# Optimization experiments

Measured on AMD Instinct MI355X. Metric: run time of the kernel, lower is better.

Reference implementation:

```python
import jax, jax.numpy as jnp
import numpy as np

H, KV, HD = 16, 8, 128           # heads, kv heads, head_dim
THETA, EPS = 1.0e6, 1e-6         # rope theta, rmsnorm eps
QMAX = 127.0                     # symmetric int8


def qdq(x):
    """Symmetric int8 fake quant-dequant along last dim (per-token / per-out-channel)."""
    s = jnp.maximum(jnp.max(jnp.abs(x), axis=-1, keepdims=True) / QMAX, 1e-8)
    q = jnp.clip(jnp.round(x / s), -QMAX, QMAX) * s
    return x + jax.lax.stop_gradient(q - x)  # STE


def rms_norm(x, w):
    v = jnp.mean(jnp.square(x.astype(jnp.float32)), axis=-1, keepdims=True)
    return (x.astype(jnp.float32) * jax.lax.rsqrt(v + EPS)).astype(x.dtype) * w


def rotate_half(x):
    x1, x2 = jnp.split(x, 2, axis=-1)
    return jnp.concatenate([-x2, x1], axis=-1)


def setup_inputs() -> dict:
    key = jax.random.key(0)
    ks = jax.random.split(key, 6)
    B, S, D = 1, 2048, 2048
    return {
        "hidden_states": jax.random.normal(ks[0], (B, S, D), jnp.float32),
        "Wq": jax.random.normal(ks[1], (H * HD, D), jnp.float32) * 0.02,
        "Wk": jax.random.normal(ks[2], (KV * HD, D), jnp.float32) * 0.02,
        "Wv": jax.random.normal(ks[3], (KV * HD, D), jnp.float32) * 0.02,
        "Wo": jax.random.normal(ks[4], (D, H * HD), jnp.float32) * 0.02,
        "q_norm_w": jnp.ones((HD,), jnp.float32),
        "k_norm_w": jnp.ones((HD,), jnp.float32),
        "position_ids": jnp.arange(S, dtype=jnp.int32)[None, :],
    }


def reference(hidden_states, Wq, Wk, Wv, Wo, q_norm_w, k_norm_w, position_ids):
    B, S, D = hidden_states.shape
    xq = qdq(hidden_states)                                  # per-token act quant (shared input)
    q = (xq @ qdq(Wq).T).reshape(B, S, H, HD).transpose(0, 2, 1, 3)   # [B,H,S,hd]
    k = (xq @ qdq(Wk).T).reshape(B, S, KV, HD).transpose(0, 2, 1, 3)  # [B,KV,S,hd]
    v = (xq @ qdq(Wv).T).reshape(B, S, KV, HD).transpose(0, 2, 1, 3)

    q = rms_norm(q, q_norm_w)
    k = rms_norm(k, k_norm_w)

    # rotary embeddings
    inv = 1.0 / (THETA ** (jnp.arange(0, HD, 2, dtype=jnp.float32) / HD))
    freqs = position_ids.astype(jnp.float32)[..., None] * inv          # [B,S,hd/2]
    emb = jnp.concatenate([freqs, freqs], axis=-1)                     # [B,S,hd]
    cos = jnp.cos(emb)[:, None].astype(q.dtype)                        # [B,1,S,hd]
    sin = jnp.sin(emb)[:, None].astype(q.dtype)
    q = q * cos + rotate_half(q) * sin
    k = k * cos + rotate_half(k) * sin

    # qkt_matmul.quant_x1 / quant_x2
    q = qdq(q)
    k = qdq(k)

    # GQA repeat
    g = H // KV
    k = jnp.repeat(k, g, axis=1)
    v = jnp.repeat(v, g, axis=1)

    scores = jnp.einsum("bhqd,bhkd->bhqk", q, k) * (HD ** -0.5)       # [B,H,S,S]
    causal = jnp.tril(jnp.ones((S, S), bool))
    scores = jnp.where(causal[None, None], scores, jnp.float32(-1e9))
    p = jax.nn.softmax(scores.astype(jnp.float32), axis=-1).astype(q.dtype)

    # pv_matmul.quant_x1 / quant_x2
    p = qdq(p)
    v = qdq(v)
    attn = jnp.einsum("bhqk,bhkd->bhqd", p, v)                        # [B,H,S,hd]
    attn = attn.transpose(0, 2, 1, 3).reshape(B, S, H * HD)
    return qdq(attn) @ qdq(Wo).T
```

## Files before the change

kernel.cpp:

```cpp
#include <hip/hip_runtime.h>
#include <math.h>

#define NH 16
#define NKV 8
#define HDIM 128
#define SEQ 2048
#define DMODEL 2048

typedef int   v4i __attribute__((ext_vector_type(4)));
typedef float v4f __attribute__((ext_vector_type(4)));
typedef __bf16 v8bf __attribute__((ext_vector_type(8)));

static constexpr float SM_SCALE = 0.08838834764831843f;

#define GLOBP(p) (__attribute__((address_space(1))) void*)(p)
#define LDSP(p)  (__attribute__((address_space(3))) void*)(p)
#define ASYNC16(g, l) __builtin_amdgcn_global_load_lds(GLOBP(g), LDSP(l), 16, 0, 0)


__global__ __launch_bounds__(256) void quant_all_k(const float* __restrict__ hidden,
        const float* __restrict__ Wq, const float* __restrict__ Wk,
        const float* __restrict__ Wv, const float* __restrict__ Wo,
        signed char* __restrict__ out, float* __restrict__ scale) {
    int p = blockIdx.x;
    int row0g = p * 16;
    const float* in; int lr0;
    if (row0g < 2048)      { in = hidden; lr0 = row0g; }
    else if (row0g < 4096) { in = Wq; lr0 = row0g - 2048; }
    else if (row0g < 5120) { in = Wk; lr0 = row0g - 4096; }
    else if (row0g < 6144) { in = Wv; lr0 = row0g - 5120; }
    else                   { in = Wo; lr0 = row0g - 6144; }
    const int cols = 2048;
    int tid = threadIdx.x;
    __shared__ float srow[16];
    int r = tid >> 4, l16 = tid & 15;
    const float4* x4 = (const float4*)(in + (size_t)(lr0 + r) * cols);
    float amax = 0.f;
    for (int c4 = l16; c4 < (cols >> 2); c4 += 16) {
        float4 v = x4[c4];
        amax = fmaxf(amax, fmaxf(fmaxf(fabsf(v.x), fabsf(v.y)),
                                 fmaxf(fabsf(v.z), fabsf(v.w))));
    }
#pragma unroll
    for (int m = 1; m <= 8; m <<= 1) amax = fmaxf(amax, __shfl_xor(amax, m));
    if (l16 == 0) {
        float s = fmaxf(amax / 127.0f, 1e-8f);
        srow[r] = s;
        scale[row0g + r] = s;
    }
    __syncthreads();
    int total = (cols >> 4) * 16;
    size_t obase = (size_t)p * 32768;
    for (int idx = tid; idx < total; idx += 256) {
        int f = idx >> 6, q = (idx >> 4) & 3, rr = idx & 15;
        const float* src = in + (size_t)(lr0 + rr) * cols + f * 64 + q * 16;
        float s = srow[rr];
        unsigned int wds[4];
#pragma unroll
        for (int g = 0; g < 4; ++g) {
            float4 v = *(const float4*)(src + g * 4);
            int b0 = (int)fminf(fmaxf(rintf(v.x / s), -127.f), 127.f);
            int b1 = (int)fminf(fmaxf(rintf(v.y / s), -127.f), 127.f);
            int b2 = (int)fminf(fmaxf(rintf(v.z / s), -127.f), 127.f);
            int b3 = (int)fminf(fmaxf(rintf(v.w / s), -127.f), 127.f);
            wds[g] = (b0 & 255) | ((b1 & 255) << 8) | ((b2 & 255) << 16) | ((b3 & 255) << 24);
        }
        *(uint4*)(out + obase + (size_t)idx * 16) =
            make_uint4(wds[0], wds[1], wds[2], wds[3]);
    }
}

__global__ __launch_bounds__(256) void row_quant_k(const float* __restrict__ in,
        signed char* __restrict__ out, float* __restrict__ scale, int cols) {
    int row0 = blockIdx.x * 16;
    int tid = threadIdx.x;
    __shared__ float srow[16];
    int r = tid >> 4, l16 = tid & 15;
    const float4* x4 = (const float4*)(in + (size_t)(row0 + r) * cols);
    float amax = 0.f;
    for (int c4 = l16; c4 < (cols >> 2); c4 += 16) {
        float4 v = x4[c4];
        amax = fmaxf(amax, fmaxf(fmaxf(fabsf(v.x), fabsf(v.y)),
                                 fmaxf(fabsf(v.z), fabsf(v.w))));
    }
#pragma unroll
    for (int m = 1; m <= 8; m <<= 1) amax = fmaxf(amax, __shfl_xor(amax, m));
    if (l16 == 0) {
        float s = fmaxf(amax / 127.0f, 1e-8f);
        srow[r] = s;
        scale[row0 + r] = s;
    }
    __syncthreads();
    int total = (cols >> 4) * 16;
    size_t obase = ((size_t)(row0 >> 4) * (cols >> 6)) << 10;
    for (int idx = tid; idx < total; idx += 256) {
        int f = idx >> 6, q = (idx >> 4) & 3, rr = idx & 15;
        const float* src = in + (size_t)(row0 + rr) * cols + f * 64 + q * 16;
        float s = srow[rr];
        unsigned int wds[4];
#pragma unroll
        for (int g = 0; g < 4; ++g) {
            float4 v = *(const float4*)(src + g * 4);
            int b0 = (int)fminf(fmaxf(rintf(v.x / s), -127.f), 127.f);
            int b1 = (int)fminf(fmaxf(rintf(v.y / s), -127.f), 127.f);
            int b2 = (int)fminf(fmaxf(rintf(v.z / s), -127.f), 127.f);
            int b3 = (int)fminf(fmaxf(rintf(v.w / s), -127.f), 127.f);
            wds[g] = (b0 & 255) | ((b1 & 255) << 8) | ((b2 & 255) << 16) | ((b3 & 255) << 24);
        }
        *(uint4*)(out + obase + (size_t)idx * 16) =
            make_uint4(wds[0], wds[1], wds[2], wds[3]);
    }
}

__global__ __launch_bounds__(256, 2) void gemm_i8_k(const signed char* __restrict__ A,
        const float* __restrict__ sa, const signed char* __restrict__ B,
        const float* __restrict__ sb, float* __restrict__ C, int M, int N, int K) {
    __shared__ __align__(16) signed char lsA[2][8192];
    __shared__ __align__(16) signed char lsB[2][8192];
    int tid = threadIdx.x;
    int w = tid >> 6, l = tid & 63;
    int wr = w >> 1, wc = w & 1;
    int lrow = l & 15;
    int m0 = blockIdx.y * 128, n0 = blockIdx.x * 128;
    int kb6 = K >> 6;
    v4i acc[4][4];
#pragma unroll
    for (int i = 0; i < 4; ++i)
#pragma unroll
        for (int j = 0; j < 4; ++j) acc[i][j] = (v4i){0, 0, 0, 0};

    auto stage = [&](int buf, int k6) {
#pragma unroll
        for (int a = 0; a < 2; ++a) {
            int f = a * 4 + w;
            ASYNC16(A + (((size_t)(((m0 >> 4) + f) * kb6 + k6)) << 10) + l * 16,
                    lsA[buf] + f * 1024);
            ASYNC16(B + (((size_t)(((n0 >> 4) + f) * kb6 + k6)) << 10) + l * 16,
                    lsB[buf] + f * 1024);
        }
    };

    stage(0, 0);
    asm volatile("s_waitcnt vmcnt(0)" ::: "memory");
    __syncthreads();
    int cur = 0;
    for (int t = 0; t < kb6; ++t) {
        if (t + 1 < kb6) stage(cur ^ 1, t + 1);
        v4i af[4], bf[4];
#pragma unroll
        for (int i = 0; i < 4; ++i) af[i] = *(const v4i*)(lsA[cur] + (wr * 4 + i) * 1024 + l * 16);
#pragma unroll
        for (int j = 0; j < 4; ++j) bf[j] = *(const v4i*)(lsB[cur] + (wc * 4 + j) * 1024 + l * 16);
#pragma unroll
        for (int i = 0; i < 4; ++i)
#pragma unroll
            for (int j = 0; j < 4; ++j)
                acc[i][j] = __builtin_amdgcn_mfma_i32_16x16x64_i8(af[i], bf[j], acc[i][j], 0, 0, 0);
        asm volatile("s_waitcnt vmcnt(0)" ::: "memory");
        __syncthreads();
        cur ^= 1;
    }
    int r0 = m0 + wr * 64, c0 = n0 + wc * 64;
    int lg = l >> 4;
    float sbv[4];
#pragma unroll
    for (int j = 0; j < 4; ++j) sbv[j] = sb[c0 + j * 16 + lrow];
#pragma unroll
    for (int i = 0; i < 4; ++i) {
        float4 s4 = *(const float4*)(sa + r0 + i * 16 + lg * 4);
        float sav[4] = {s4.x, s4.y, s4.z, s4.w};
#pragma unroll
        for (int j = 0; j < 4; ++j) {
#pragma unroll
            for (int reg = 0; reg < 4; ++reg) {
                int rr = r0 + i * 16 + lg * 4 + reg;
                C[(size_t)rr * N + c0 + j * 16 + lrow] = (float)acc[i][j][reg] * (sav[reg] * sbv[j]);
            }
        }
    }
}

__global__ void rope_init_k(float* __restrict__ inv_tab) {
    int i = threadIdx.x;
    inv_tab[i] = 1.0f / (float)pow(1.0e6, (double)i / 64.0);
}
__global__ void rope_tab_k(const int* __restrict__ pos_ids, const float* __restrict__ inv_tab,
                           float* __restrict__ ct, float* __restrict__ st) {
    int t = blockIdx.x;
    int fi = threadIdx.x;
    float fr = (float)pos_ids[t] * inv_tab[fi];
    float sn, c;
    sincosf(fr, &sn, &c);
    ct[t * 64 + fi] = c;
    st[t * 64 + fi] = sn;
}

__global__ __launch_bounds__(256) void qkv_post_k(const float* __restrict__ qkv_lin,
        const float* __restrict__ qw, const float* __restrict__ kw,
        const float* __restrict__ ct, const float* __restrict__ st,
        signed char* __restrict__ q_i8, float* __restrict__ sq,
        signed char* __restrict__ k_i8, float* __restrict__ sk,
        float* __restrict__ v_dq) {
    int t = blockIdx.x;
    int wv = threadIdx.x >> 6, l = threadIdx.x & 63;
    const float* row = qkv_lin + (size_t)t * 4096;
    float cth = ct[t * 64 + l];
    float sth = st[t * 64 + l];
    size_t ta0 = (size_t)(((t >> 4) * 2) << 10)
               + (size_t)((((l >> 4) & 3) << 8) + ((t & 15) << 4) + (l & 15));
    for (int slot = wv; slot < 32; slot += 4) {
        float x0 = row[slot * 128 + l];
        float x1 = row[slot * 128 + l + 64];
        if (slot < 24) {
            float ss = x0 * x0 + x1 * x1;
#pragma unroll
            for (int m = 1; m <= 32; m <<= 1) ss += __shfl_xor(ss, m);
            float rs = 1.0f / sqrtf(ss / 128.0f + 1e-6f);
            const float* wn = (slot < 16) ? qw : kw;
            x0 = (x0 * rs) * wn[l];
            x1 = (x1 * rs) * wn[l + 64];
            float nx0 = x0 * cth - x1 * sth;
            float nx1 = x1 * cth + x0 * sth;
            x0 = nx0; x1 = nx1;
        }
        float amax = fmaxf(fabsf(x0), fabsf(x1));
#pragma unroll
        for (int m = 1; m <= 32; m <<= 1) amax = fmaxf(amax, __shfl_xor(amax, m));
        float s = fmaxf(amax / 127.0f, 1e-8f);
        float q0 = fminf(fmaxf(rintf(x0 / s), -127.f), 127.f);
        float q1 = fminf(fmaxf(rintf(x1 / s), -127.f), 127.f);
        if (slot < 16) {
            signed char* dst = q_i8 + (size_t)slot * (SEQ * 128);
            dst[ta0] = (signed char)(int)q0;
            dst[ta0 + 1024] = (signed char)(int)q1;
            if (l == 0) sq[slot * SEQ + t] = s;
        } else if (slot < 24) {
            signed char* dst = k_i8 + (size_t)(slot - 16) * (SEQ * 128);
            dst[ta0] = (signed char)(int)q0;
            dst[ta0 + 1024] = (signed char)(int)q1;
            if (l == 0) sk[(slot - 16) * SEQ + t] = s;
        } else {
            float* dst = v_dq + ((size_t)(slot - 24) * SEQ + t) * HDIM;
            dst[l] = q0 * s;
            dst[l + 64] = q1 * s;
        }
    }
}

__device__ __forceinline__ unsigned int f2bf(float x) {
    unsigned int u = __float_as_uint(x);
    return (u + 0x7fffu + ((u >> 16) & 1u)) >> 16;
}
__device__ __forceinline__ float bf2f(unsigned int h) {
    return __uint_as_float(h << 16);
}

__global__ __launch_bounds__(256) void vt_split_k(const float* __restrict__ v_dq,
        unsigned short* __restrict__ vtT) {
    int kv = blockIdx.y, kb = blockIdx.x;
    int t0 = kb * 64;
    __shared__ float tile[64][132];
    int tid = threadIdx.x;
    const float* src = v_dq + ((size_t)kv * SEQ + t0) * HDIM;
#pragma unroll
    for (int i = 0; i < 8; ++i) {
        int f4 = i * 256 + tid;
        int r = f4 >> 5, c = (f4 & 31) << 2;
        float4 v = *(const float4*)(src + r * HDIM + c);
        tile[r][c] = v.x; tile[r][c + 1] = v.y; tile[r][c + 2] = v.z; tile[r][c + 3] = v.w;
    }
    __syncthreads();
    int d = tid >> 1, th = (tid & 1) * 32;
    size_t base_hi = (size_t)(kv * 2 + 0) * (SEQ * 128);
    size_t base_lo = (size_t)(kv * 2 + 1) * (SEQ * 128);
#pragma unroll
    for (int j = 0; j < 32; j += 2) {
        int tl = th + j;
        float a = tile[tl][d], b = tile[tl + 1][d];
        unsigned int ah = f2bf(a), bh = f2bf(b);
        unsigned int al = f2bf(a - bf2f(ah)), bl = f2bf(b - bf2f(bh));
        int off = kb * 8192 + ((d >> 4) * 2 + ((tl >> 5) & 1)) * 512
                + (((d & 15) + (((tl >> 3) & 3) << 4)) << 3) + (tl & 7);
        *(unsigned int*)(vtT + base_hi + off) = ah | (bh << 16);
        *(unsigned int*)(vtT + base_lo + off) = al | (bl << 16);
    }
}

__global__ __launch_bounds__(256, 4) void attn_p1_k(const signed char* __restrict__ q_i8,
        const float* __restrict__ sq, const signed char* __restrict__ k_i8,
        const float* __restrict__ sk, float* __restrict__ mm) {
    int bx = blockIdx.x, hp = blockIdx.y;
    int qb = 31 - (bx >> 2), c = bx & 3;
    int nch = (qb + 8) >> 3;
    if (c >= nch) return;
    int q0 = qb * 64;
    int kb0 = c * 8, kb1 = min((c + 1) * 8, qb + 1);
    int tid = threadIdx.x, w = tid >> 6, l = tid & 63;
    int lrow = l & 15, lg = l >> 4;
    int h0 = hp * 2, h1 = h0 + 1;

    const signed char* qtA = q_i8 + (size_t)h0 * (SEQ * 128)
                           + ((size_t)((((q0 >> 4) + w) * 2)) << 10) + l * 16;
    const signed char* qtB = qtA + (size_t)(SEQ * 128);
    v4i qfA0 = *(const v4i*)(qtA), qfA1 = *(const v4i*)(qtA + 1024);
    v4i qfB0 = *(const v4i*)(qtB), qfB1 = *(const v4i*)(qtB + 1024);
    float4 sA = *(const float4*)(sq + (size_t)h0 * SEQ + q0 + w * 16 + lg * 4);
    float4 sB = *(const float4*)(sq + (size_t)h1 * SEQ + q0 + w * 16 + lg * 4);
    float sqrA[4] = {sA.x, sA.y, sA.z, sA.w};
    float sqrB[4] = {sB.x, sB.y, sB.z, sB.w};
    const signed char* kbase = k_i8 + (size_t)hp * (SEQ * 128);
    const float* skb = sk + (size_t)hp * SEQ;

    float mA[4], mB[4];
#pragma unroll
    for (int r = 0; r < 4; ++r) { mA[r] = -1e30f; mB[r] = -1e30f; }

    v4i ka[8], kn[8];
    float skc[4], skn[4];
    auto loadK = [&](v4i* dst, float* sdst, int k0) {
#pragma unroll
        for (int f = 0; f < 8; ++f)
            dst[f] = *(const v4i*)(kbase + ((size_t)((k0 >> 4) * 2 + f) << 10) + l * 16);
#pragma unroll
        for (int j = 0; j < 4; ++j) sdst[j] = skb[k0 + j * 16 + lrow];
    };

    loadK(ka, skc, kb0 * 64);
    for (int kb = kb0; kb < kb1; ++kb) {
        if (kb + 1 < kb1) loadK(kn, skn, (kb + 1) * 64);
        int k0 = kb * 64;
        v4i sciA[4], sciB[4];
#pragma unroll
        for (int j = 0; j < 4; ++j) {
            v4i z = {0, 0, 0, 0};
            v4i tA = __builtin_amdgcn_mfma_i32_16x16x64_i8(qfA0, ka[j * 2], z, 0, 0, 0);
            sciA[j] = __builtin_amdgcn_mfma_i32_16x16x64_i8(qfA1, ka[j * 2 + 1], tA, 0, 0, 0);
            v4i tB = __builtin_amdgcn_mfma_i32_16x16x64_i8(qfB0, ka[j * 2], z, 0, 0, 0);
            sciB[j] = __builtin_amdgcn_mfma_i32_16x16x64_i8(qfB1, ka[j * 2 + 1], tB, 0, 0, 0);
        }
#pragma unroll
        for (int reg = 0; reg < 4; ++reg) {
            int r = q0 + w * 16 + lg * 4 + reg;
#pragma unroll
            for (int j = 0; j < 4; ++j) {
                bool ok = (k0 + j * 16 + lrow <= r);
                float ss = skc[j] * SM_SCALE;
                float svA = ((float)sciA[j][reg] * sqrA[reg]) * ss;
                float svB = ((float)sciB[j][reg] * sqrB[reg]) * ss;
                mA[reg] = fmaxf(mA[reg], ok ? svA : -1e30f);
                mB[reg] = fmaxf(mB[reg], ok ? svB : -1e30f);
            }
        }
        if (kb + 1 < kb1) {
#pragma unroll
            for (int f = 0; f < 8; ++f) ka[f] = kn[f];
#pragma unroll
            for (int j = 0; j < 4; ++j) skc[j] = skn[j];
        }
    }
#pragma unroll
    for (int reg = 0; reg < 4; ++reg) {
#pragma unroll
        for (int mask = 1; mask <= 8; mask <<= 1) {
            mA[reg] = fmaxf(mA[reg], __shfl_xor(mA[reg], mask));
            mB[reg] = fmaxf(mB[reg], __shfl_xor(mB[reg], mask));
        }
    }
    if (lrow == 0) {
        size_t bA = ((size_t)(h0 * 32 + qb) * 4 + c) * 64;
        size_t bB = ((size_t)(h1 * 32 + qb) * 4 + c) * 64;
#pragma unroll
        for (int reg = 0; reg < 4; ++reg) {
            mm[bA + w * 16 + lg * 4 + reg] = mA[reg];
            mm[bB + w * 16 + lg * 4 + reg] = mB[reg];
        }
    }
}


__global__ __launch_bounds__(256, 2) void attn_p2_k(const signed char* __restrict__ q_i8,
        const float* __restrict__ sq, const signed char* __restrict__ k_i8,
        const float* __restrict__ sk, const unsigned short* __restrict__ vtT,
        const float* __restrict__ mm, float* __restrict__ attn2, float* __restrict__ pp,
        float* __restrict__ zb) {
    __shared__ __align__(16) unsigned short vlds[2][16384];
    __shared__ __align__(16) signed char klds[8192];
    __shared__ __align__(16) unsigned short plds[4096];
    int bx = blockIdx.x, hp = blockIdx.y;
    int qb = 31 - (bx >> 1), c = bx & 1;
    int nch2 = (qb >= 16) ? 2 : 1;
    if (c >= nch2) return;
    int q0 = qb * 64;
    int kb0 = c * 16, kb1 = min((c + 1) * 16, qb + 1);
    int tid = threadIdx.x, w = tid >> 6, l = tid & 63;
    int lrow = l & 15, lg = l >> 4;
    int h0 = hp * 2, h1 = h0 + 1;

    const signed char* qtA = q_i8 + (size_t)h0 * (SEQ * 128)
                           + ((size_t)((((q0 >> 4) + w) * 2)) << 10) + l * 16;
    const signed char* qtB = qtA + (size_t)(SEQ * 128);
    v4i qfA0 = *(const v4i*)(qtA), qfA1 = *(const v4i*)(qtA + 1024);
    v4i qfB0 = *(const v4i*)(qtB), qfB1 = *(const v4i*)(qtB + 1024);
    float4 sA = *(const float4*)(sq + (size_t)h0 * SEQ + q0 + w * 16 + lg * 4);
    float4 sB = *(const float4*)(sq + (size_t)h1 * SEQ + q0 + w * 16 + lg * 4);
    float sqrA[4] = {sA.x, sA.y, sA.z, sA.w};
    float sqrB[4] = {sB.x, sB.y, sB.z, sB.w};

    int nch1 = (qb + 8) >> 3;
    float mfA[4], mfB[4];
#pragma unroll
    for (int reg = 0; reg < 4; ++reg) {
        int r = w * 16 + lg * 4 + reg;
        float MA = -1e30f, MB = -1e30f;
        for (int c1 = 0; c1 < nch1; ++c1) {
            MA = fmaxf(MA, mm[((size_t)(h0 * 32 + qb) * 4 + c1) * 64 + r]);
            MB = fmaxf(MB, mm[((size_t)(h1 * 32 + qb) * 4 + c1) * 64 + r]);
        }
        mfA[reg] = MA; mfB[reg] = MB;
    }

    const signed char* kbase = k_i8 + (size_t)hp * (SEQ * 128);
    const float* skb = sk + (size_t)hp * SEQ;
    const unsigned short* vt_h = vtT + (size_t)(hp * 2 + 0) * (SEQ * 128);
    const unsigned short* vt_l = vtT + (size_t)(hp * 2 + 1) * (SEQ * 128);

    auto issueV = [&](int kb) {
        unsigned short* vb = &vlds[kb & 1][0];
#pragma unroll
        for (int a = 0; a < 8; ++a) {
            int fv = a * 4 + w;
            int sp_ = fv >> 4, fr = fv & 15;
            const unsigned short* vsrc = (sp_ ? vt_l : vt_h) + kb * 8192 + fr * 512 + l * 8;
            ASYNC16(vsrc, vb + fv * 512);
        }
    };
    auto issueK = [&](int kb) {
#pragma unroll
        for (int a = 0; a < 2; ++a) {
            int f = a * 4 + w;
            ASYNC16(kbase + ((size_t)(kb * 8 + f) << 10) + l * 16, klds + f * 1024);
        }
    };

    v4f accA[8], accB[8];
#pragma unroll
    for (int jd = 0; jd < 8; ++jd) {
        accA[jd] = (v4f){0.f, 0.f, 0.f, 0.f};
        accB[jd] = (v4f){0.f, 0.f, 0.f, 0.f};
    }
    float ztA[4] = {0.f, 0.f, 0.f, 0.f};
    float ztB[4] = {0.f, 0.f, 0.f, 0.f};

    issueV(kb0);
    issueK(kb0);
    asm volatile("s_waitcnt vmcnt(0)" ::: "memory");
    __syncthreads();
    for (int kb = kb0; kb < kb1; ++kb) {
        int k0 = kb * 64;
        v4i ka[8];
#pragma unroll
        for (int f = 0; f < 8; ++f)
            ka[f] = *(const v4i*)(klds + f * 1024 + l * 16);
        float skc[4];
#pragma unroll
        for (int j = 0; j < 4; ++j) skc[j] = skb[k0 + j * 16 + lrow];
        __syncthreads();
        if (kb + 1 < kb1) {
            issueV(kb + 1);
            issueK(kb + 1);
        }
        v4i sciA[4], sciB[4];
#pragma unroll
        for (int j = 0; j < 4; ++j) {
            v4i z = {0, 0, 0, 0};
            v4i tA = __builtin_amdgcn_mfma_i32_16x16x64_i8(qfA0, ka[j * 2], z, 0, 0, 0);
            sciA[j] = __builtin_amdgcn_mfma_i32_16x16x64_i8(qfA1, ka[j * 2 + 1], tA, 0, 0, 0);
            v4i tB = __builtin_amdgcn_mfma_i32_16x16x64_i8(qfB0, ka[j * 2], z, 0, 0, 0);
            sciB[j] = __builtin_amdgcn_mfma_i32_16x16x64_i8(qfB1, ka[j * 2 + 1], tB, 0, 0, 0);
        }
#pragma unroll
        for (int reg = 0; reg < 4; ++reg) {
            int rq = lg * 4 + reg;
            int r = q0 + w * 16 + rq;
#pragma unroll
            for (int j = 0; j < 4; ++j) {
                int cc = j * 16 + lrow;
                float pd = 0.f;
                if (k0 + cc <= r) {
                    float sv = ((float)sciA[j][reg] * (sqrA[reg] * skc[j])) * SM_SCALE;
                    float e = __expf(sv - mfA[reg]);
                    ztA[reg] += e;
                    pd = fminf(rintf(127.0f * e), 127.f);
                }
                plds[(w * 2 + (cc >> 5)) * 512 + (rq + 16 * ((cc >> 3) & 3)) * 8 + (cc & 7)] =
                    (unsigned short)(__float_as_uint(pd) >> 16);
            }
        }
        v8bf pfA0 = *(const v8bf*)(plds + (w * 2 + 0) * 512 + l * 8);
        v8bf pfA1 = *(const v8bf*)(plds + (w * 2 + 1) * 512 + l * 8);
#pragma unroll
        for (int reg = 0; reg < 4; ++reg) {
            int rq = lg * 4 + reg;
            int r = q0 + w * 16 + rq;
#pragma unroll
            for (int j = 0; j < 4; ++j) {
                int cc = j * 16 + lrow;
                float pd = 0.f;
                if (k0 + cc <= r) {
                    float sv = ((float)sciB[j][reg] * (sqrB[reg] * skc[j])) * SM_SCALE;
                    float e = __expf(sv - mfB[reg]);
                    ztB[reg] += e;
                    pd = fminf(rintf(127.0f * e), 127.f);
                }
                plds[(w * 2 + (cc >> 5)) * 512 + (rq + 16 * ((cc >> 3) & 3)) * 8 + (cc & 7)] =
                    (unsigned short)(__float_as_uint(pd) >> 16);
            }
        }
        v8bf pfB0 = *(const v8bf*)(plds + (w * 2 + 0) * 512 + l * 8);
        v8bf pfB1 = *(const v8bf*)(plds + (w * 2 + 1) * 512 + l * 8);
        const unsigned short* vb = &vlds[kb & 1][0];
#pragma unroll
        for (int jd = 0; jd < 8; ++jd) {
            v8bf vh0 = *(const v8bf*)(vb + (jd * 2 + 0) * 512 + l * 8);
            v8bf vh1 = *(const v8bf*)(vb + (jd * 2 + 1) * 512 + l * 8);
            v8bf vl0 = *(const v8bf*)(vb + (16 + jd * 2 + 0) * 512 + l * 8);
            v8bf vl1 = *(const v8bf*)(vb + (16 + jd * 2 + 1) * 512 + l * 8);
            v4f tA = accA[jd];
            tA = __builtin_amdgcn_mfma_f32_16x16x32_bf16(pfA0, vh0, tA, 0, 0, 0);
            tA = __builtin_amdgcn_mfma_f32_16x16x32_bf16(pfA1, vh1, tA, 0, 0, 0);
            tA = __builtin_amdgcn_mfma_f32_16x16x32_bf16(pfA0, vl0, tA, 0, 0, 0);
            tA = __builtin_amdgcn_mfma_f32_16x16x32_bf16(pfA1, vl1, tA, 0, 0, 0);
            accA[jd] = tA;
            v4f tB = accB[jd];
            tB = __builtin_amdgcn_mfma_f32_16x16x32_bf16(pfB0, vh0, tB, 0, 0, 0);
            tB = __builtin_amdgcn_mfma_f32_16x16x32_bf16(pfB1, vh1, tB, 0, 0, 0);
            tB = __builtin_amdgcn_mfma_f32_16x16x32_bf16(pfB0, vl0, tB, 0, 0, 0);
            tB = __builtin_amdgcn_mfma_f32_16x16x32_bf16(pfB1, vl1, tB, 0, 0, 0);
            accB[jd] = tB;
        }
        asm volatile("s_waitcnt vmcnt(0)" ::: "memory");
        __syncthreads();
    }
#pragma unroll
    for (int reg = 0; reg < 4; ++reg) {
#pragma unroll
        for (int mask = 1; mask <= 8; mask <<= 1) {
            ztA[reg] += __shfl_xor(ztA[reg], mask);
            ztB[reg] += __shfl_xor(ztB[reg], mask);
        }
    }
    if (qb < 16) {
        float spA[4], spB[4];
#pragma unroll
        for (int reg = 0; reg < 4; ++reg) {
            spA[reg] = fmaxf((1.0f / ztA[reg]) / 127.0f, 1e-8f);
            spB[reg] = fmaxf((1.0f / ztB[reg]) / 127.0f, 1e-8f);
        }
#pragma unroll
        for (int jd = 0; jd < 8; ++jd)
#pragma unroll
            for (int reg = 0; reg < 4; ++reg) {
                int r = q0 + w * 16 + lg * 4 + reg;
                attn2[(size_t)r * DMODEL + h0 * HDIM + jd * 16 + lrow] = accA[jd][reg] * spA[reg];
                attn2[(size_t)r * DMODEL + h1 * HDIM + jd * 16 + lrow] = accB[jd][reg] * spB[reg];
            }
    } else {
        if (c == 0) {
#pragma unroll
            for (int jd = 0; jd < 8; ++jd)
#pragma unroll
                for (int reg = 0; reg < 4; ++reg) {
                    int r = q0 + w * 16 + lg * 4 + reg;
                    attn2[(size_t)r * DMODEL + h0 * HDIM + jd * 16 + lrow] = accA[jd][reg];
                    attn2[(size_t)r * DMODEL + h1 * HDIM + jd * 16 + lrow] = accB[jd][reg];
                }
        } else {
#pragma unroll
            for (int jd = 0; jd < 8; ++jd)
#pragma unroll
                for (int reg = 0; reg < 4; ++reg) {
                    int rr = w * 16 + lg * 4 + reg;
                    pp[(((size_t)h0 * 16 + (qb - 16)) * 64 + rr) * 128 + jd * 16 + lrow] = accA[jd][reg];
                    pp[(((size_t)h1 * 16 + (qb - 16)) * 64 + rr) * 128 + jd * 16 + lrow] = accB[jd][reg];
                }
        }
        if (lrow == 0) {
            size_t zA = (((size_t)h0 * 16 + (qb - 16)) * 2 + c) * 64;
            size_t zB = (((size_t)h1 * 16 + (qb - 16)) * 2 + c) * 64;
#pragma unroll
            for (int reg = 0; reg < 4; ++reg) {
                zb[zA + w * 16 + lg * 4 + reg] = ztA[reg];
                zb[zB + w * 16 + lg * 4 + reg] = ztB[reg];
            }
        }
    }
}

__global__ __launch_bounds__(256) void attn_red_k(float* __restrict__ attn2,
        const float* __restrict__ pp, const float* __restrict__ zb) {
    int t16 = blockIdx.x, h = blockIdx.y;
    int qb = t16 + 16;
    int tid = threadIdx.x;
    for (int e = tid; e < 2048; e += 256) {
        int i = (e * 4) >> 7, j = (e * 4) & 127;
        float z0 = zb[(((size_t)h * 16 + t16) * 2 + 0) * 64 + i];
        float z1 = zb[(((size_t)h * 16 + t16) * 2 + 1) * 64 + i];
        float zinv = 1.0f / (z0 + z1);
        float spv = fmaxf(zinv / 127.0f, 1e-8f);
        float4 p = *(const float4*)&pp[(((size_t)h * 16 + t16) * 64 + i) * 128 + j];
        float* d = &attn2[(size_t)(qb * 64 + i) * DMODEL + h * HDIM + j];
        float4 dv = *(float4*)d;
        dv.x = (dv.x + p.x) * spv; dv.y = (dv.y + p.y) * spv;
        dv.z = (dv.z + p.z) * spv; dv.w = (dv.w + p.w) * spv;
        *(float4*)d = dv;
    }
}

extern "C" void kernel_launch(void* const* d_in, const int* in_sizes, int n_in,
                              void* d_out, int out_size, void* d_ws, size_t ws_size,
                              hipStream_t stream) {
    (void)in_sizes; (void)n_in; (void)out_size; (void)ws_size;
    const float* hidden = (const float*)d_in[0];
    const float* Wq = (const float*)d_in[1];
    const float* Wk = (const float*)d_in[2];
    const float* Wv = (const float*)d_in[3];
    const float* Wo = (const float*)d_in[4];
    const float* qw = (const float*)d_in[5];
    const float* kw = (const float*)d_in[6];
    const int* pos = (const int*)d_in[7];
    float* out = (float*)d_out;
    char* ws = (char*)d_ws;

    const size_t MB = 1024 * 1024;
    signed char* x_i8  = (signed char*)(ws);
    signed char* wq_i8 = (signed char*)(ws + 4 * MB);
    signed char* wo_i8 = (signed char*)(ws + 12 * MB);
    signed char* q_i8  = (signed char*)(ws + 16 * MB);
    signed char* k_i8  = (signed char*)(ws + 20 * MB);
    float* sx  = (float*)(ws + 22 * MB);
    float* swq = sx + 2048;
    float* swo = sx + 6144;
    float* sq  = sx + 8192;
    float* sk  = sq + NH * SEQ;
    float* sa  = sk + NKV * SEQ;
    float* inv_tab = sa + 2048;
    float* ct  = (float*)(ws + 22 * MB + 512 * 1024);
    float* st  = (float*)(ws + 22 * MB + 1024 * 1024);
    float* qkv_lin = (float*)(ws + 24 * MB);
    unsigned short* vtT = (unsigned short*)(ws + 24 * MB);
    float* attn2 = (float*)(ws + 32 * MB);
    float* pp    = (float*)(ws + 48 * MB);
    float* v_dq  = (float*)(ws + 56 * MB);
    float* mm    = (float*)(ws + 56 * MB);
    float* zb    = (float*)(ws + 56 * MB + 512 * 1024);
    signed char* a_i8 = x_i8;

    rope_init_k<<<1, 64, 0, stream>>>(inv_tab);
    rope_tab_k<<<2048, 64, 0, stream>>>(pos, inv_tab, ct, st);
    quant_all_k<<<512, 256, 0, stream>>>(hidden, Wq, Wk, Wv, Wo, x_i8, sx);

    gemm_i8_k<<<dim3(32, 16), 256, 0, stream>>>(x_i8, sx, wq_i8, swq, qkv_lin, 2048, 4096, 2048);

    qkv_post_k<<<2048, 256, 0, stream>>>(qkv_lin, qw, kw, ct, st, q_i8, sq, k_i8, sk, v_dq);
    vt_split_k<<<dim3(32, 8), 256, 0, stream>>>(v_dq, vtT);

    attn_p1_k<<<dim3(128, 8), 256, 0, stream>>>(q_i8, sq, k_i8, sk, mm);
    attn_p2_k<<<dim3(64, 8), 256, 0, stream>>>(q_i8, sq, k_i8, sk, vtT, mm, attn2, pp, zb);
    attn_red_k<<<dim3(16, 16), 256, 0, stream>>>(attn2, pp, zb);

    row_quant_k<<<128, 256, 0, stream>>>(attn2, a_i8, sa, 2048);
    gemm_i8_k<<<dim3(16, 16), 256, 0, stream>>>(a_i8, sa, wo_i8, swo, out, 2048, 2048, 2048);
}
```

Baseline: 202.5 us.

## Use single fp16 V and P operands in PV matmul instead of split bf16

```diff
diff --git a/kernel.cpp b/kernel.cpp
--- a/kernel.cpp
+++ b/kernel.cpp
@@ -9,7 +9,7 @@
 
 typedef int   v4i __attribute__((ext_vector_type(4)));
 typedef float v4f __attribute__((ext_vector_type(4)));
-typedef __bf16 v8bf __attribute__((ext_vector_type(8)));
+typedef _Float16 v8h __attribute__((ext_vector_type(8)));
 
 static constexpr float SM_SCALE = 0.08838834764831843f;
 
@@ -17,6 +17,11 @@
 #define LDSP(p)  (__attribute__((address_space(3))) void*)(p)
 #define ASYNC16(g, l) __builtin_amdgcn_global_load_lds(GLOBP(g), LDSP(l), 16, 0, 0)
 
+
+__device__ __forceinline__ unsigned short f2h_bits(float x) {
+    _Float16 h = (_Float16)x;
+    return __builtin_bit_cast(unsigned short, h);
+}
 
 __global__ __launch_bounds__(256) void quant_all_k(const float* __restrict__ hidden,
         const float* __restrict__ Wq, const float* __restrict__ Wk,
@@ -199,8 +204,7 @@
         const float* __restrict__ qw, const float* __restrict__ kw,
         const float* __restrict__ ct, const float* __restrict__ st,
         signed char* __restrict__ q_i8, float* __restrict__ sq,
-        signed char* __restrict__ k_i8, float* __restrict__ sk,
-        float* __restrict__ v_dq) {
+        signed char* __restrict__ k_i8, float* __restrict__ sk) {
     int t = blockIdx.x;
     int wv = threadIdx.x >> 6, l = threadIdx.x & 63;
     const float* row = qkv_lin + (size_t)t * 4096;
@@ -208,21 +212,19 @@
     float sth = st[t * 64 + l];
     size_t ta0 = (size_t)(((t >> 4) * 2) << 10)
                + (size_t)((((l >> 4) & 3) << 8) + ((t & 15) << 4) + (l & 15));
-    for (int slot = wv; slot < 32; slot += 4) {
+    for (int slot = wv; slot < 24; slot += 4) {
         float x0 = row[slot * 128 + l];
         float x1 = row[slot * 128 + l + 64];
-        if (slot < 24) {
-            float ss = x0 * x0 + x1 * x1;
-#pragma unroll
-            for (int m = 1; m <= 32; m <<= 1) ss += __shfl_xor(ss, m);
-            float rs = 1.0f / sqrtf(ss / 128.0f + 1e-6f);
-            const float* wn = (slot < 16) ? qw : kw;
-            x0 = (x0 * rs) * wn[l];
-            x1 = (x1 * rs) * wn[l + 64];
-            float nx0 = x0 * cth - x1 * sth;
-            float nx1 = x1 * cth + x0 * sth;
-            x0 = nx0; x1 = nx1;
-        }
+        float ss = x0 * x0 + x1 * x1;
+#pragma unroll
+        for (int m = 1; m <= 32; m <<= 1) ss += __shfl_xor(ss, m);
+        float rs = 1.0f / sqrtf(ss / 128.0f + 1e-6f);
+        const float* wn = (slot < 16) ? qw : kw;
+        x0 = (x0 * rs) * wn[l];
+        x1 = (x1 * rs) * wn[l + 64];
+        float nx0 = x0 * cth - x1 * sth;
+        float nx1 = x1 * cth + x0 * sth;
+        x0 = nx0; x1 = nx1;
         float amax = fmaxf(fabsf(x0), fabsf(x1));
 #pragma unroll
         for (int m = 1; m <= 32; m <<= 1) amax = fmaxf(amax, __shfl_xor(amax, m));
@@ -234,55 +236,53 @@
             dst[ta0] = (signed char)(int)q0;
             dst[ta0 + 1024] = (signed char)(int)q1;
             if (l == 0) sq[slot * SEQ + t] = s;
-        } else if (slot < 24) {
+        } else {
             signed char* dst = k_i8 + (size_t)(slot - 16) * (SEQ * 128);
             dst[ta0] = (signed char)(int)q0;
             dst[ta0 + 1024] = (signed char)(int)q1;
             if (l == 0) sk[(slot - 16) * SEQ + t] = s;
-        } else {
-            float* dst = v_dq + ((size_t)(slot - 24) * SEQ + t) * HDIM;
-            dst[l] = q0 * s;
-            dst[l + 64] = q1 * s;
-        }
-    }
-}
-
-__device__ __forceinline__ unsigned int f2bf(float x) {
-    unsigned int u = __float_as_uint(x);
-    return (u + 0x7fffu + ((u >> 16) & 1u)) >> 16;
-}
-__device__ __forceinline__ float bf2f(unsigned int h) {
-    return __uint_as_float(h << 16);
-}
-
-__global__ __launch_bounds__(256) void vt_split_k(const float* __restrict__ v_dq,
+        }
+    }
+}
+
+__global__ __launch_bounds__(256) void vt_split_k(const float* __restrict__ qkv_lin,
         unsigned short* __restrict__ vtT) {
     int kv = blockIdx.y, kb = blockIdx.x;
     int t0 = kb * 64;
     __shared__ float tile[64][132];
+    __shared__ float srow[64];
     int tid = threadIdx.x;
-    const float* src = v_dq + ((size_t)kv * SEQ + t0) * HDIM;
+    const float* src = qkv_lin + (size_t)t0 * 4096 + 3072 + kv * 128;
 #pragma unroll
     for (int i = 0; i < 8; ++i) {
         int f4 = i * 256 + tid;
         int r = f4 >> 5, c = (f4 & 31) << 2;
-        float4 v = *(const float4*)(src + r * HDIM + c);
+        float4 v = *(const float4*)(src + (size_t)r * 4096 + c);
         tile[r][c] = v.x; tile[r][c + 1] = v.y; tile[r][c + 2] = v.z; tile[r][c + 3] = v.w;
+    }
+    __syncthreads();
+    {
+        int r = tid >> 2, qq = tid & 3;
+        float amax = 0.f;
+#pragma unroll
+        for (int e = 0; e < 32; ++e) amax = fmaxf(amax, fabsf(tile[r][qq * 32 + e]));
+        amax = fmaxf(amax, __shfl_xor(amax, 1));
+        amax = fmaxf(amax, __shfl_xor(amax, 2));
+        if (qq == 0) srow[r] = fmaxf(amax / 127.0f, 1e-8f);
     }
     __syncthreads();
     int d = tid >> 1, th = (tid & 1) * 32;
-    size_t base_hi = (size_t)(kv * 2 + 0) * (SEQ * 128);
-    size_t base_lo = (size_t)(kv * 2 + 1) * (SEQ * 128);
+    size_t base = (size_t)kv * (SEQ * 128);
 #pragma unroll
     for (int j = 0; j < 32; j += 2) {
         int tl = th + j;
-        float a = tile[tl][d], b = tile[tl + 1][d];
-        unsigned int ah = f2bf(a), bh = f2bf(b);
-        unsigned int al = f2bf(a - bf2f(ah)), bl = f2bf(b - bf2f(bh));
+        float s0 = srow[tl], s1 = srow[tl + 1];
+        float a = fminf(fmaxf(rintf(tile[tl][d] / s0), -127.f), 127.f) * s0;
+        float b = fminf(fmaxf(rintf(tile[tl + 1][d] / s1), -127.f), 127.f) * s1;
+        unsigned int ua = f2h_bits(a), ub = f2h_bits(b);
         int off = kb * 8192 + ((d >> 4) * 2 + ((tl >> 5) & 1)) * 512
                 + (((d & 15) + (((tl >> 3) & 3) << 4)) << 3) + (tl & 7);
-        *(unsigned int*)(vtT + base_hi + off) = ah | (bh << 16);
-        *(unsigned int*)(vtT + base_lo + off) = al | (bl << 16);
+        *(unsigned int*)(vtT + base + off) = ua | (ub << 16);
     }
 }
 
@@ -377,13 +377,12 @@
     }
 }
 
-
-__global__ __launch_bounds__(256, 2) void attn_p2_k(const signed char* __restrict__ q_i8,
+__global__ __launch_bounds__(256, 3) void attn_p2_k(const signed char* __restrict__ q_i8,
         const float* __restrict__ sq, const signed char* __restrict__ k_i8,
         const float* __restrict__ sk, const unsigned short* __restrict__ vtT,
         const float* __restrict__ mm, float* __restrict__ attn2, float* __restrict__ pp,
         float* __restrict__ zb) {
-    __shared__ __align__(16) unsigned short vlds[2][16384];
+    __shared__ __align__(16) unsigned short vlds[2][8192];
     __shared__ __align__(16) signed char klds[8192];
     __shared__ __align__(16) unsigned short plds[4096];
     int bx = blockIdx.x, hp = blockIdx.y;
@@ -421,17 +420,14 @@
 
     const signed char* kbase = k_i8 + (size_t)hp * (SEQ * 128);
     const float* skb = sk + (size_t)hp * SEQ;
-    const unsigned short* vt_h = vtT + (size_t)(hp * 2 + 0) * (SEQ * 128);
-    const unsigned short* vt_l = vtT + (size_t)(hp * 2 + 1) * (SEQ * 128);
+    const unsigned short* vt = vtT + (size_t)hp * (SEQ * 128);
 
     auto issueV = [&](int kb) {
         unsigned short* vb = &vlds[kb & 1][0];
 #pragma unroll
-        for (int a = 0; a < 8; ++a) {
+        for (int a = 0; a < 4; ++a) {
             int fv = a * 4 + w;
-            int sp_ = fv >> 4, fr = fv & 15;
-            const unsigned short* vsrc = (sp_ ? vt_l : vt_h) + kb * 8192 + fr * 512 + l * 8;
-            ASYNC16(vsrc, vb + fv * 512);
+            ASYNC16(vt + (size_t)kb * 8192 + fv * 512 + l * 8, vb + fv * 512);
         }
     };
     auto issueK = [&](int kb) {
@@ -493,11 +489,11 @@
                     pd = fminf(rintf(127.0f * e), 127.f);
                 }
                 plds[(w * 2 + (cc >> 5)) * 512 + (rq + 16 * ((cc >> 3) & 3)) * 8 + (cc & 7)] =
-                    (unsigned short)(__float_as_uint(pd) >> 16);
+                    f2h_bits(pd);
             }
         }
-        v8bf pfA0 = *(const v8bf*)(plds + (w * 2 + 0) * 512 + l * 8);
-        v8bf pfA1 = *(const v8bf*)(plds + (w * 2 + 1) * 512 + l * 8);
+        v8h pfA0 = *(const v8h*)(plds + (w * 2 + 0) * 512 + l * 8);
+        v8h pfA1 = *(const v8h*)(plds + (w * 2 + 1) * 512 + l * 8);
 #pragma unroll
         for (int reg = 0; reg < 4; ++reg) {
             int rq = lg * 4 + reg;
@@ -513,29 +509,23 @@
                     pd = fminf(rintf(127.0f * e), 127.f);
                 }
                 plds[(w * 2 + (cc >> 5)) * 512 + (rq + 16 * ((cc >> 3) & 3)) * 8 + (cc & 7)] =
-                    (unsigned short)(__float_as_uint(pd) >> 16);
+                    f2h_bits(pd);
             }
         }
-        v8bf pfB0 = *(const v8bf*)(plds + (w * 2 + 0) * 512 + l * 8);
-        v8bf pfB1 = *(const v8bf*)(plds + (w * 2 + 1) * 512 + l * 8);
+        v8h pfB0 = *(const v8h*)(plds + (w * 2 + 0) * 512 + l * 8);
+        v8h pfB1 = *(const v8h*)(plds + (w * 2 + 1) * 512 + l * 8);
         const unsigned short* vb = &vlds[kb & 1][0];
 #pragma unroll
         for (int jd = 0; jd < 8; ++jd) {
-            v8bf vh0 = *(const v8bf*)(vb + (jd * 2 + 0) * 512 + l * 8);
-            v8bf vh1 = *(const v8bf*)(vb + (jd * 2 + 1) * 512 + l * 8);
-            v8bf vl0 = *(const v8bf*)(vb + (16 + jd * 2 + 0) * 512 + l * 8);
-            v8bf vl1 = *(const v8bf*)(vb + (16 + jd * 2 + 1) * 512 + l * 8);
+            v8h vh0 = *(const v8h*)(vb + (jd * 2 + 0) * 512 + l * 8);
+            v8h vh1 = *(const v8h*)(vb + (jd * 2 + 1) * 512 + l * 8);
             v4f tA = accA[jd];
-            tA = __builtin_amdgcn_mfma_f32_16x16x32_bf16(pfA0, vh0, tA, 0, 0, 0);
-            tA = __builtin_amdgcn_mfma_f32_16x16x32_bf16(pfA1, vh1, tA, 0, 0, 0);
-            tA = __builtin_amdgcn_mfma_f32_16x16x32_bf16(pfA0, vl0, tA, 0, 0, 0);
-            tA = __builtin_amdgcn_mfma_f32_16x16x32_bf16(pfA1, vl1, tA, 0, 0, 0);
+            tA = __builtin_amdgcn_mfma_f32_16x16x32_f16(pfA0, vh0, tA, 0, 0, 0);
+            tA = __builtin_amdgcn_mfma_f32_16x16x32_f16(pfA1, vh1, tA, 0, 0, 0);
             accA[jd] = tA;
             v4f tB = accB[jd];
-            tB = __builtin_amdgcn_mfma_f32_16x16x32_bf16(pfB0, vh0, tB, 0, 0, 0);
-            tB = __builtin_amdgcn_mfma_f32_16x16x32_bf16(pfB1, vh1, tB, 0, 0, 0);
-            tB = __builtin_amdgcn_mfma_f32_16x16x32_bf16(pfB0, vl0, tB, 0, 0, 0);
-            tB = __builtin_amdgcn_mfma_f32_16x16x32_bf16(pfB1, vl1, tB, 0, 0, 0);
+            tB = __builtin_amdgcn_mfma_f32_16x16x32_f16(pfB0, vh0, tB, 0, 0, 0);
+            tB = __builtin_amdgcn_mfma_f32_16x16x32_f16(pfB1, vh1, tB, 0, 0, 0);
             accB[jd] = tB;
         }
         asm volatile("s_waitcnt vmcnt(0)" ::: "memory");
@@ -647,12 +637,11 @@
     float* ct  = (float*)(ws + 22 * MB + 512 * 1024);
     float* st  = (float*)(ws + 22 * MB + 1024 * 1024);
     float* qkv_lin = (float*)(ws + 24 * MB);
-    unsigned short* vtT = (unsigned short*)(ws + 24 * MB);
     float* attn2 = (float*)(ws + 32 * MB);
     float* pp    = (float*)(ws + 48 * MB);
-    float* v_dq  = (float*)(ws + 56 * MB);
-    float* mm    = (float*)(ws + 56 * MB);
-    float* zb    = (float*)(ws + 56 * MB + 512 * 1024);
+    unsigned short* vtT = (unsigned short*)(ws + 56 * MB);
+    float* mm    = (float*)(ws + 60 * MB);
+    float* zb    = (float*)(ws + 60 * MB + 512 * 1024);
     signed char* a_i8 = x_i8;
 
     rope_init_k<<<1, 64, 0, stream>>>(inv_tab);
@@ -661,8 +650,8 @@
 
     gemm_i8_k<<<dim3(32, 16), 256, 0, stream>>>(x_i8, sx, wq_i8, swq, qkv_lin, 2048, 4096, 2048);
 
-    qkv_post_k<<<2048, 256, 0, stream>>>(qkv_lin, qw, kw, ct, st, q_i8, sq, k_i8, sk, v_dq);
-    vt_split_k<<<dim3(32, 8), 256, 0, stream>>>(v_dq, vtT);
+    qkv_post_k<<<2048, 256, 0, stream>>>(qkv_lin, qw, kw, ct, st, q_i8, sq, k_i8, sk);
+    vt_split_k<<<dim3(32, 8), 256, 0, stream>>>(qkv_lin, vtT);
 
     attn_p1_k<<<dim3(128, 8), 256, 0, stream>>>(q_i8, sq, k_i8, sk, mm);
     attn_p2_k<<<dim3(64, 8), 256, 0, stream>>>(q_i8, sq, k_i8, sk, vtT, mm, attn2, pp, zb);
```

After: 212.4 us. +4.9%, slower.
